# Kernel tuning notes

Hardware: AMD Instinct MI355X
Metric: run time of the kernel (lower is better)

The kernel has to match this reference:

```python
import jax, jax.numpy as jnp
import numpy as np

GRAPH_BIAS_SCALE = 0.7
COMMITMENT_COST = 0.25
DECAY = 0.995
EPS = 1e-6

N_TOKENS = 32768
LATENT = 512
N_SYMBOLS = 8192
EMBED_DIM = 2 * LATENT


def setup_inputs() -> dict:
    key = jax.random.key(0)
    ks = jax.random.split(key, 6)
    return {
        "z_real": jax.random.normal(ks[0], (N_TOKENS, LATENT), jnp.float32),
        "z_imag": jax.random.normal(ks[1], (N_TOKENS, LATENT), jnp.float32),
        "prev_symbol_idx": jax.random.randint(ks[2], (N_TOKENS,), 0, N_SYMBOLS, jnp.int64),
        "codebook": jax.random.normal(ks[3], (N_SYMBOLS, EMBED_DIM), jnp.float32),
        "cluster_size": jax.random.uniform(ks[4], (N_SYMBOLS,), jnp.float32),
        "embed_avg": jax.random.normal(ks[5], (N_SYMBOLS, EMBED_DIM), jnp.float32),
        "adjacency": jax.random.normal(jax.random.fold_in(key, 7), (N_SYMBOLS, N_SYMBOLS), jnp.float32),
    }


def reference(z_real, z_imag, prev_symbol_idx, codebook, cluster_size, embed_avg, adjacency):
    n_symbols = codebook.shape[0]
    z_flat = jnp.concatenate([z_real, z_imag], axis=-1)  # [N, 2*latent]

    # squared-distance matrix via matmul expansion: [N, n_symbols]
    d = (jnp.sum(z_flat ** 2, axis=1, keepdims=True)
         + jnp.sum(codebook ** 2, axis=1)
         - 2.0 * z_flat @ codebook.T)

    # graph-adjacency prior bias (row gather + sigmoid)
    bias = GRAPH_BIAS_SCALE * jax.nn.sigmoid(adjacency[prev_symbol_idx])
    d = d - bias

    min_indices = jnp.argmin(d, axis=1)          # [N]
    z_q = codebook[min_indices]                  # gather, pre-EMA codebook

    # --- EMA codebook update (training mode), scatter via segment_sum ---
    ones = jnp.ones(min_indices.shape, jnp.float32)
    counts = jax.ops.segment_sum(ones, min_indices, num_segments=n_symbols)
    new_cluster_size = cluster_size * DECAY + counts * (1.0 - DECAY)
    embed_sum = jax.ops.segment_sum(jax.lax.stop_gradient(z_flat), min_indices,
                                    num_segments=n_symbols)
    new_embed_avg = embed_avg * DECAY + embed_sum * (1.0 - DECAY)
    n_total = jnp.sum(new_cluster_size)
    cs = (new_cluster_size + EPS) / (n_total + n_symbols * EPS) * n_total
    new_codebook = new_embed_avg / cs[:, None]

    # --- losses and straight-through estimator ---
    loss_vq = jnp.mean((z_q - jax.lax.stop_gradient(z_flat)) ** 2)
    loss_commit = jnp.mean((jax.lax.stop_gradient(z_q) - z_flat) ** 2)
    loss = loss_vq + COMMITMENT_COST * loss_commit

    z_q_st = z_flat + jax.lax.stop_gradient(z_q - z_flat)
    D = z_real.shape[-1]
    z_complex = jax.lax.complex(z_q_st[..., :D], z_q_st[..., D:])

    return z_complex, loss, min_indices, new_codebook, new_cluster_size, new_embed_avg
```

## Files before the change

kernel.cpp:

```cpp
#include <hip/hip_runtime.h>
#include <math.h>
#include <float.h>

#define M_TOK   32768
#define NSYM    8192
#define KDIM    1024
#define LAT     512

#define DECAY_F 0.995f
#define OMD_F   0.005f
#define GBS_F   0.7f
#define EPS_F   1e-6f
#define WIN_F   3.0f

typedef unsigned short u16;
typedef unsigned int   u32;
typedef short short8 __attribute__((ext_vector_type(8)));
typedef float f32x4  __attribute__((ext_vector_type(4)));

#define GLOAD_LDS16(g, l) \
    __builtin_amdgcn_global_load_lds((const __attribute__((address_space(1))) u32*)(g), \
                                     (__attribute__((address_space(3))) u32*)(l), 16, 0, 0)

__device__ __forceinline__ u16 f2bf(float f) {
    u32 u = __float_as_uint(f);
    return (u16)((u + 0x7FFF + ((u >> 16) & 1)) >> 16);
}

__global__ void k_convA(const float* __restrict__ zr, const float* __restrict__ zi,
                        u16* __restrict__ A) {
    size_t t = (size_t)blockIdx.x * 256 + threadIdx.x;
    size_t base = t * 8;
    int tok = (int)(base >> 10);
    int k0  = (int)(base & 1023);
    const float* src = (k0 < 512) ? zr + (size_t)tok * 512 + k0
                                  : zi + (size_t)tok * 512 + (k0 - 512);
    float4 f0 = *(const float4*)src;
    float4 f1 = *(const float4*)(src + 4);
    u32 q0 = f2bf(f0.x) | ((u32)f2bf(f0.y) << 16);
    u32 q1 = f2bf(f0.z) | ((u32)f2bf(f0.w) << 16);
    u32 q2 = f2bf(f1.x) | ((u32)f2bf(f1.y) << 16);
    u32 q3 = f2bf(f1.z) | ((u32)f2bf(f1.w) << 16);
    *(uint4*)&A[base] = make_uint4(q0, q1, q2, q3);
}

__global__ void k_convB(const float* __restrict__ cb, u16* __restrict__ B,
                        float* __restrict__ cnorm) {
    size_t t = (size_t)blockIdx.x * 256 + threadIdx.x;
    size_t base = t * 8;
    float4 f0 = *(const float4*)&cb[base];
    float4 f1 = *(const float4*)&cb[base + 4];
    u32 q0 = f2bf(f0.x) | ((u32)f2bf(f0.y) << 16);
    u32 q1 = f2bf(f0.z) | ((u32)f2bf(f0.w) << 16);
    u32 q2 = f2bf(f1.x) | ((u32)f2bf(f1.y) << 16);
    u32 q3 = f2bf(f1.z) | ((u32)f2bf(f1.w) << 16);
    *(uint4*)&B[base] = make_uint4(q0, q1, q2, q3);
    float nrm = f0.x * f0.x + f0.y * f0.y + f0.z * f0.z + f0.w * f0.w
              + f1.x * f1.x + f1.y * f1.y + f1.z * f1.z + f1.w * f1.w;
#pragma unroll
    for (int m = 32; m; m >>= 1) nrm += __shfl_xor(nrm, m, 64);
    __shared__ float part[4];
    int lane = threadIdx.x & 63, w = threadIdx.x >> 6;
    if (lane == 0) part[w] = nrm;
    __syncthreads();
    if (threadIdx.x == 0)   cnorm[blockIdx.x * 2]     = part[0] + part[1];
    if (threadIdx.x == 128) cnorm[blockIdx.x * 2 + 1] = part[2] + part[3];
}

__global__ __launch_bounds__(256, 4) void k_screen(
    const u16* __restrict__ Ah, const u16* __restrict__ Bh,
    const float* __restrict__ cnorm,
    float* __restrict__ candV, u16* __restrict__ candI)
{
    __shared__ __align__(16) unsigned char smA[16384];
    __shared__ __align__(16) unsigned char smB[16384];
    __shared__ float smv[128][2][2];
    __shared__ float smi[128][2];

    const int sblk = (blockIdx.x & 7) * 128 + (blockIdx.x >> 3);
    const int bx = sblk >> 2;
    const int by = sblk & 3;

    const int tid  = threadIdx.x;
    const int lane = tid & 63;
    const int w    = tid >> 6;
    const int wr   = w >> 1, wc = w & 1;
    const int row0 = bx * 128;
    const int sBase = w * 256;

    for (int cc = 0; cc < 16; ++cc) {
        const int chunk = by * 16 + cc;
        const int colBase = chunk * 128;

        f32x4 acc[4][4];
#pragma unroll
        for (int m = 0; m < 4; ++m)
#pragma unroll
            for (int n = 0; n < 4; ++n) acc[m][n] = (f32x4){0.f, 0.f, 0.f, 0.f};

        for (int ks = 0; ks < 16; ++ks) {
            const int kk0 = ks * 64;
            __syncthreads();
#pragma unroll
            for (int i = 0; i < 4; ++i) {
                int slot = sBase + i * 64 + lane;
                int r = slot >> 3;
                int c = (slot & 7) ^ (r & 7);
                const u16* ga = Ah + ((size_t)(row0 + r) * KDIM + kk0 + c * 8);
                GLOAD_LDS16(ga, smA + (size_t)(sBase + i * 64) * 16);
                const u16* gb = Bh + ((size_t)(colBase + r) * KDIM + kk0 + c * 8);
                GLOAD_LDS16(gb, smB + (size_t)(sBase + i * 64) * 16);
            }
            __syncthreads();
#pragma unroll
            for (int h = 0; h < 2; ++h) {
                short8 af[4], bfr[4];
#pragma unroll
                for (int m = 0; m < 4; ++m) {
                    int r = wr * 64 + m * 16 + (lane & 15);
                    int byte = r * 128 + h * 64 + (lane >> 4) * 16;
                    byte ^= (r & 7) << 4;
                    af[m] = *(const short8*)(smA + byte);
                }
#pragma unroll
                for (int n = 0; n < 4; ++n) {
                    int r = wc * 64 + n * 16 + (lane & 15);
                    int byte = r * 128 + h * 64 + (lane >> 4) * 16;
                    byte ^= (r & 7) << 4;
                    bfr[n] = *(const short8*)(smB + byte);
                }
#pragma unroll
                for (int m = 0; m < 4; ++m)
#pragma unroll
                    for (int n = 0; n < 4; ++n)
                        acc[m][n] = __builtin_amdgcn_mfma_f32_16x16x32_bf16(
                            af[m], bfr[n], acc[m][n], 0, 0, 0);
            }
        }

        float cn[4];
#pragma unroll
        for (int n = 0; n < 4; ++n)
            cn[n] = cnorm[colBase + wc * 64 + n * 16 + (lane & 15)];

#pragma unroll
        for (int m = 0; m < 4; ++m)
#pragma unroll
            for (int j = 0; j < 4; ++j) {
                int rowL = wr * 64 + m * 16 + (lane >> 4) * 4 + j;
                float v1 = INFINITY, v2 = INFINITY, i1v = 0.f;
#pragma unroll
                for (int n = 0; n < 4; ++n) {
                    float s = cn[n] - 2.0f * acc[m][n][j];
                    float ci = (float)(colBase + wc * 64 + n * 16 + (lane & 15));
                    if (s < v1) { v2 = v1; v1 = s; i1v = ci; }
                    else v2 = fminf(v2, s);
                }
#pragma unroll
                for (int msk = 1; msk < 16; msk <<= 1) {
                    float o1 = __shfl_xor(v1, msk, 16);
                    float oi = __shfl_xor(i1v, msk, 16);
                    float o2 = __shfl_xor(v2, msk, 16);
                    float n2 = fminf(fminf(v2, o2), fmaxf(v1, o1));
                    if (o1 < v1) { v1 = o1; i1v = oi; }
                    v2 = n2;
                }
                if ((lane & 15) == 0) {
                    smv[rowL][wc][0] = v1;  smv[rowL][wc][1] = v2;
                    smi[rowL][wc] = i1v;
                }
            }
        __syncthreads();
        {
            int half = tid >> 7;
            int row  = tid & 127;
            float v1 = smv[row][half][0], v2 = smv[row][half][1];
            float iv = smi[row][half];
            size_t tcol = (size_t)(row0 + row);
            int halfIdx = chunk * 2 + half;
            candV[(size_t)(halfIdx * 2 + 0) * M_TOK + tcol] = v1;
            candV[(size_t)(halfIdx * 2 + 1) * M_TOK + tcol] = v2;
            candI[(size_t)halfIdx * M_TOK + tcol]           = (u16)iv;
        }
    }
}

__global__ void k_zero(u32* __restrict__ counts, u32* __restrict__ cursors,
                       float* __restrict__ out_loss) {
    int i = blockIdx.x * 256 + threadIdx.x;
    if (i < NSYM) { counts[i] = 0; cursors[i] = 0; }
    if (i == 0) out_loss[0] = 0.0f;
}

#define SEL_TOK 32
__device__ __forceinline__ void rescore(
    const float* __restrict__ codebook, const float* __restrict__ adjacency,
    const double* zreg, int prw, int col, int lane, double& bestS, int& bestI)
{
    const float* crow = codebook + (size_t)col * KDIM;
    double dot = 0.0, cn2 = 0.0;
#pragma unroll
    for (int j = 0; j < 16; ++j) {
        double c = (double)crow[lane + 64 * j];
        dot += c * zreg[j]; cn2 += c * c;
    }
#pragma unroll
    for (int m = 32; m; m >>= 1) {
        dot += __shfl_xor(dot, m, 64);
        cn2 += __shfl_xor(cn2, m, 64);
    }
    double a = (double)adjacency[(size_t)prw * NSYM + col];
    double sc = cn2 - 2.0 * dot - (double)GBS_F / (1.0 + exp(-a));
    if (sc < bestS || (sc == bestS && col < bestI)) { bestS = sc; bestI = col; }
}

__global__ __launch_bounds__(256) void k_select(
    const float* __restrict__ zr, const float* __restrict__ zi,
    const int* __restrict__ prev,
    const float* __restrict__ codebook,
    const float* __restrict__ adjacency,
    const float* __restrict__ candV, const u16* __restrict__ candI,
    float* __restrict__ out_idx, u32* __restrict__ counts)
{
    __shared__ float sv[256][SEL_TOK + 1];
    __shared__ u16   si[128][SEL_TOK + 2];
    const int tok0 = blockIdx.x * SEL_TOK;
    const int w = threadIdx.x >> 6, lane = threadIdx.x & 63;

    for (int idx = threadIdx.x; idx < 256 * SEL_TOK; idx += 256) {
        int e = idx >> 5, t = idx & (SEL_TOK - 1);
        sv[e][t] = candV[(size_t)e * M_TOK + tok0 + t];
    }
    for (int idx = threadIdx.x; idx < 128 * SEL_TOK; idx += 256) {
        int e = idx >> 5, t = idx & (SEL_TOK - 1);
        si[e][t] = candI[(size_t)e * M_TOK + tok0 + t];
    }
    __syncthreads();

    for (int tt = 0; tt < SEL_TOK / 4; ++tt) {
        const int t = w * (SEL_TOK / 4) + tt;
        const int tok = tok0 + t;
        float va1 = sv[4 * lane + 0][t];
        float va2 = sv[4 * lane + 1][t];
        float vb1 = sv[4 * lane + 2][t];
        float vb2 = sv[4 * lane + 3][t];
        int   ia  = (int)si[2 * lane + 0][t];
        int   ib  = (int)si[2 * lane + 1][t];

        float mm = fminf(va1, vb1);
#pragma unroll
        for (int m = 32; m; m >>= 1) mm = fminf(mm, __shfl_xor(mm, m, 64));
        const float thr = mm + WIN_F;

        unsigned long long m1a = __ballot(va1 <= thr);
        unsigned long long m1b = __ballot(vb1 <= thr);
        unsigned long long mha = __ballot(va2 <= thr);
        unsigned long long mhb = __ballot(vb2 <= thr);

        int bestI;
        if ((mha | mhb) == 0 && __popcll(m1a) + __popcll(m1b) == 1) {
            if (m1a) bestI = __shfl(ia, __ffsll(m1a) - 1, 64);
            else     bestI = __shfl(ib, __ffsll(m1b) - 1, 64);
        } else {
            double zreg[16];
#pragma unroll
            for (int j = 0; j < 8; ++j)
                zreg[j] = (double)zr[(size_t)tok * LAT + lane + 64 * j];
#pragma unroll
            for (int j = 0; j < 8; ++j)
                zreg[8 + j] = (double)zi[(size_t)tok * LAT + lane + 64 * j];
            const int prw = prev[tok];

            double bestS = DBL_MAX; bestI = 0x7FFFFFFF;
            unsigned long long sa = m1a & ~mha, sb = m1b & ~mhb;
            while (sa) { int c = __ffsll(sa) - 1; sa &= sa - 1;
                rescore(codebook, adjacency, zreg, prw, __shfl(ia, c, 64), lane, bestS, bestI); }
            while (sb) { int c = __ffsll(sb) - 1; sb &= sb - 1;
                rescore(codebook, adjacency, zreg, prw, __shfl(ib, c, 64), lane, bestS, bestI); }
            while (mha) { int c = __ffsll(mha) - 1; mha &= mha - 1;
                for (int q = 0; q < 64; ++q)
                    rescore(codebook, adjacency, zreg, prw, c * 128 + q, lane, bestS, bestI); }
            while (mhb) { int c = __ffsll(mhb) - 1; mhb &= mhb - 1;
                for (int q = 0; q < 64; ++q)
                    rescore(codebook, adjacency, zreg, prw, c * 128 + 64 + q, lane, bestS, bestI); }
        }
        if (lane == 0) {
            out_idx[tok] = (float)bestI;
            atomicAdd(&counts[bestI], 1u);
        }
    }
}

__global__ __launch_bounds__(1024) void k_scan(
    const u32* __restrict__ counts, const float* __restrict__ cs_old,
    float* __restrict__ out_cs, u32* __restrict__ offsets,
    float* __restrict__ scal)
{
    const int tid = threadIdx.x;
    const int lane = tid & 63, w = tid >> 6;
    const int base = tid * 8;
    u32 c[8], pre[8], T = 0;
#pragma unroll
    for (int q = 0; q < 8; ++q) { c[q] = counts[base + q]; pre[q] = T; T += c[q]; }
    u32 inc = T;
#pragma unroll
    for (int d = 1; d < 64; d <<= 1) {
        u32 v = __shfl_up(inc, d, 64);
        if (lane >= d) inc += v;
    }
    __shared__ u32 wt[16];
    if (lane == 63) wt[w] = inc;
    __syncthreads();
    if (tid < 16) {
        u32 v = wt[tid];
#pragma unroll
        for (int d = 1; d < 16; d <<= 1) {
            u32 o = __shfl_up(v, d, 16);
            if (tid >= d) v += o;
        }
        wt[tid] = v;
    }
    __syncthreads();
    u32 ex = (w ? wt[w - 1] : 0) + inc - T;
#pragma unroll
    for (int q = 0; q < 8; ++q) offsets[base + q] = ex + pre[q];

    float nt = 0.0f;
#pragma unroll
    for (int q = 0; q < 8; ++q) {
        float ncs = cs_old[base + q] * DECAY_F + OMD_F * (float)c[q];
        out_cs[base + q] = ncs;
        nt += ncs;
    }
#pragma unroll
    for (int m = 32; m; m >>= 1) nt += __shfl_xor(nt, m, 64);
    __shared__ float red[16];
    if (lane == 0) red[w] = nt;
    __syncthreads();
    if (tid == 0) {
        float s = 0.0f;
#pragma unroll
        for (int i = 0; i < 16; ++i) s += red[i];
        scal[0] = s;
        scal[1] = s + (float)NSYM * EPS_F;
    }
}

__global__ void k_place(const float* __restrict__ idxf, const u32* __restrict__ offsets,
                        u32* __restrict__ cursors, u32* __restrict__ list) {
    int t = blockIdx.x * 256 + threadIdx.x;
    int s = (int)idxf[t];
    u32 slot = atomicAdd(&cursors[s], 1u);
    list[offsets[s] + slot] = (u32)t;
}

__global__ __launch_bounds__(256) void k_emit(
    const float* __restrict__ zr, const float* __restrict__ zi,
    const float* __restrict__ embed_avg,
    const u32* __restrict__ counts, const u32* __restrict__ offsets,
    const u32* __restrict__ list, const float* __restrict__ out_cs,
    const float* __restrict__ scal,
    float* __restrict__ out_ea, float* __restrict__ out_cb)
{
    const int s = blockIdx.x;
    const u32 cnt = counts[s], off = offsets[s];
    const int j = threadIdx.x * 4;
    float a0 = 0.f, a1 = 0.f, a2 = 0.f, a3 = 0.f;
    for (u32 n = 0; n < cnt; ++n) {
        int t = (int)list[off + n];
        const float* src = (j < 512) ? zr + (size_t)t * 512 + j
                                     : zi + (size_t)t * 512 + (j - 512);
        float4 v = *(const float4*)src;
        a0 += v.x; a1 += v.y; a2 += v.z; a3 += v.w;
    }
    float4 ea = *(const float4*)&embed_avg[(size_t)s * KDIM + j];
    float4 nea = make_float4(ea.x * DECAY_F + a0 * OMD_F,
                             ea.y * DECAY_F + a1 * OMD_F,
                             ea.z * DECAY_F + a2 * OMD_F,
                             ea.w * DECAY_F + a3 * OMD_F);
    *(float4*)&out_ea[(size_t)s * KDIM + j] = nea;
    float ntot = scal[0], denom = scal[1];
    float cs = (out_cs[s] + EPS_F) / denom * ntot;
    float inv = 1.0f / cs;
    *(float4*)&out_cb[(size_t)s * KDIM + j] =
        make_float4(nea.x * inv, nea.y * inv, nea.z * inv, nea.w * inv);
}

__global__ __launch_bounds__(256) void k_zq(
    const float* __restrict__ zr, const float* __restrict__ zi,
    const float* __restrict__ codebook, const float* __restrict__ idxf,
    float* __restrict__ out_zc, float* __restrict__ out_loss, int interleaved)
{
    const int w = threadIdx.x >> 6, lane = threadIdx.x & 63;
    const int tok = blockIdx.x * 4 + w;
    const int mi = (int)idxf[tok];
    const int j0 = lane * 8;
    float4 re0 = *(const float4*)&codebook[(size_t)mi * KDIM + j0];
    float4 re1 = *(const float4*)&codebook[(size_t)mi * KDIM + j0 + 4];
    float4 im0 = *(const float4*)&codebook[(size_t)mi * KDIM + LAT + j0];
    float4 im1 = *(const float4*)&codebook[(size_t)mi * KDIM + LAT + j0 + 4];
    float4 zr0 = *(const float4*)&zr[(size_t)tok * LAT + j0];
    float4 zr1 = *(const float4*)&zr[(size_t)tok * LAT + j0 + 4];
    float4 zi0 = *(const float4*)&zi[(size_t)tok * LAT + j0];
    float4 zi1 = *(const float4*)&zi[(size_t)tok * LAT + j0 + 4];
    if (interleaved) {
        float2* dst = (float2*)out_zc + (size_t)tok * LAT + j0;
        dst[0] = make_float2(re0.x, im0.x); dst[1] = make_float2(re0.y, im0.y);
        dst[2] = make_float2(re0.z, im0.z); dst[3] = make_float2(re0.w, im0.w);
        dst[4] = make_float2(re1.x, im1.x); dst[5] = make_float2(re1.y, im1.y);
        dst[6] = make_float2(re1.z, im1.z); dst[7] = make_float2(re1.w, im1.w);
    } else {
        *(float4*)&out_zc[(size_t)tok * LAT + j0]     = re0;
        *(float4*)&out_zc[(size_t)tok * LAT + j0 + 4] = re1;
    }
    float l = 0.f;
    l += (re0.x-zr0.x)*(re0.x-zr0.x) + (re0.y-zr0.y)*(re0.y-zr0.y)
       + (re0.z-zr0.z)*(re0.z-zr0.z) + (re0.w-zr0.w)*(re0.w-zr0.w);
    l += (re1.x-zr1.x)*(re1.x-zr1.x) + (re1.y-zr1.y)*(re1.y-zr1.y)
       + (re1.z-zr1.z)*(re1.z-zr1.z) + (re1.w-zr1.w)*(re1.w-zr1.w);
    l += (im0.x-zi0.x)*(im0.x-zi0.x) + (im0.y-zi0.y)*(im0.y-zi0.y)
       + (im0.z-zi0.z)*(im0.z-zi0.z) + (im0.w-zi0.w)*(im0.w-zi0.w);
    l += (im1.x-zi1.x)*(im1.x-zi1.x) + (im1.y-zi1.y)*(im1.y-zi1.y)
       + (im1.z-zi1.z)*(im1.z-zi1.z) + (im1.w-zi1.w)*(im1.w-zi1.w);
#pragma unroll
    for (int m = 32; m; m >>= 1) l += __shfl_xor(l, m, 64);
    if (lane == 0) atomicAdd(out_loss, l);
}

__global__ void k_fin(float* __restrict__ out_loss) {
    out_loss[0] = out_loss[0] * 1.25f / 33554432.0f;
}

extern "C" void kernel_launch(void* const* d_in, const int* in_sizes, int n_in,
                              void* d_out, int out_size, void* d_ws, size_t ws_size,
                              hipStream_t stream) {
    const float* z_real     = (const float*)d_in[0];
    const float* z_imag     = (const float*)d_in[1];
    const int*   prev_idx   = (const int*)d_in[2];
    const float* codebook   = (const float*)d_in[3];
    const float* cluster_sz = (const float*)d_in[4];
    const float* embed_avg  = (const float*)d_in[5];
    const float* adjacency  = (const float*)d_in[6];

    float* out = (float*)d_out;

    const size_t REST = 1 + (size_t)M_TOK + (size_t)NSYM * KDIM + NSYM
                      + (size_t)NSYM * KDIM;
    size_t zc_n = (size_t)out_size - REST;
    const size_t n_z = (size_t)M_TOK * LAT;
    int interleaved = (zc_n >= 2 * n_z) ? 1 : 0;

    float* out_zc   = out;
    float* out_loss = out + zc_n;
    float* out_idx  = out + zc_n + 1;
    float* out_cb   = out + zc_n + 1 + M_TOK;
    float* out_cs   = out_cb + (size_t)NSYM * KDIM;
    float* out_ea   = out_cs + NSYM;

    u16*   A_hi  = (u16*)out_zc;
    u16*   B_hi  = (u16*)out_cb;
    float* cnorm = out_cb + 4194304;
    float* candV = out_ea;
    u16*   candI = (u16*)(out_cb + 4202496);

    u32*   counts  = (u32*)out_zc;
    u32*   cursors = counts + NSYM;
    u32*   offsets = cursors + NSYM;
    u32*   list    = offsets + NSYM;
    float* scal    = (float*)(list + M_TOK);

    k_convA<<<16384, 256, 0, stream>>>(z_real, z_imag, A_hi);
    k_convB<<<4096, 256, 0, stream>>>(codebook, B_hi, cnorm);
    k_screen<<<1024, 256, 0, stream>>>(A_hi, B_hi, cnorm, candV, candI);
    k_zero<<<32, 256, 0, stream>>>(counts, cursors, out_loss);
    k_select<<<M_TOK / SEL_TOK, 256, 0, stream>>>(z_real, z_imag, prev_idx,
                                                  codebook, adjacency,
                                                  candV, candI, out_idx, counts);
    k_scan<<<1, 1024, 0, stream>>>(counts, cluster_sz, out_cs, offsets, scal);
    k_place<<<M_TOK / 256, 256, 0, stream>>>(out_idx, offsets, cursors, list);
    k_emit<<<NSYM, 256, 0, stream>>>(z_real, z_imag, embed_avg, counts, offsets,
                                     list, out_cs, scal, out_ea, out_cb);
    k_zq<<<M_TOK / 4, 256, 0, stream>>>(z_real, z_imag, codebook, out_idx,
                                        out_zc, out_loss, interleaved);
    k_fin<<<1, 1, 0, stream>>>(out_loss);
}
```

Measured before the change: 1.502 ms.

## Split candidate selection into fast path and queued block-parallel exact rescore

Token selection now runs in two kernels. A fast kernel resolves tokens whose bf16 screen yields a single clear candidate and appends every other token to a global work queue. A slow kernel then rescoring each queued token in FP64 with a whole block, spreading its candidate list over four wavefronts instead of one wave doing the work serially, and falls back to a full codebook scan when there are too many candidates. The screening window is also narrowed from 3.0 to 2.5, which cuts rescoring work but makes it more likely that the true argmin is excluded by bf16 screening error.

```diff
diff --git a/kernel.cpp b/kernel.cpp
--- a/kernel.cpp
+++ b/kernel.cpp
@@ -11,7 +11,7 @@
 #define OMD_F   0.005f
 #define GBS_F   0.7f
 #define EPS_F   1e-6f
-#define WIN_F   3.0f
+#define WIN_F   2.5f
 
 typedef unsigned short u16;
 typedef unsigned int   u32;
@@ -186,41 +186,17 @@
 }
 
 __global__ void k_zero(u32* __restrict__ counts, u32* __restrict__ cursors,
-                       float* __restrict__ out_loss) {
+                       u32* __restrict__ qcount, float* __restrict__ out_loss) {
     int i = blockIdx.x * 256 + threadIdx.x;
     if (i < NSYM) { counts[i] = 0; cursors[i] = 0; }
-    if (i == 0) out_loss[0] = 0.0f;
+    if (i == 0) { out_loss[0] = 0.0f; qcount[0] = 0; }
 }
 
 #define SEL_TOK 32
-__device__ __forceinline__ void rescore(
-    const float* __restrict__ codebook, const float* __restrict__ adjacency,
-    const double* zreg, int prw, int col, int lane, double& bestS, int& bestI)
-{
-    const float* crow = codebook + (size_t)col * KDIM;
-    double dot = 0.0, cn2 = 0.0;
-#pragma unroll
-    for (int j = 0; j < 16; ++j) {
-        double c = (double)crow[lane + 64 * j];
-        dot += c * zreg[j]; cn2 += c * c;
-    }
-#pragma unroll
-    for (int m = 32; m; m >>= 1) {
-        dot += __shfl_xor(dot, m, 64);
-        cn2 += __shfl_xor(cn2, m, 64);
-    }
-    double a = (double)adjacency[(size_t)prw * NSYM + col];
-    double sc = cn2 - 2.0 * dot - (double)GBS_F / (1.0 + exp(-a));
-    if (sc < bestS || (sc == bestS && col < bestI)) { bestS = sc; bestI = col; }
-}
-
-__global__ __launch_bounds__(256) void k_select(
-    const float* __restrict__ zr, const float* __restrict__ zi,
-    const int* __restrict__ prev,
-    const float* __restrict__ codebook,
-    const float* __restrict__ adjacency,
+__global__ __launch_bounds__(256) void k_select_fast(
     const float* __restrict__ candV, const u16* __restrict__ candI,
-    float* __restrict__ out_idx, u32* __restrict__ counts)
+    float* __restrict__ out_idx, u32* __restrict__ counts,
+    u32* __restrict__ qcount, u32* __restrict__ queue)
 {
     __shared__ float sv[256][SEL_TOK + 1];
     __shared__ u16   si[128][SEL_TOK + 2];
@@ -244,8 +220,6 @@
         float va2 = sv[4 * lane + 1][t];
         float vb1 = sv[4 * lane + 2][t];
         float vb2 = sv[4 * lane + 3][t];
-        int   ia  = (int)si[2 * lane + 0][t];
-        int   ib  = (int)si[2 * lane + 1][t];
 
         float mm = fminf(va1, vb1);
 #pragma unroll
@@ -254,40 +228,122 @@
 
         unsigned long long m1a = __ballot(va1 <= thr);
         unsigned long long m1b = __ballot(vb1 <= thr);
-        unsigned long long mha = __ballot(va2 <= thr);
-        unsigned long long mhb = __ballot(vb2 <= thr);
-
-        int bestI;
-        if ((mha | mhb) == 0 && __popcll(m1a) + __popcll(m1b) == 1) {
-            if (m1a) bestI = __shfl(ia, __ffsll(m1a) - 1, 64);
-            else     bestI = __shfl(ib, __ffsll(m1b) - 1, 64);
-        } else {
-            double zreg[16];
-#pragma unroll
-            for (int j = 0; j < 8; ++j)
-                zreg[j] = (double)zr[(size_t)tok * LAT + lane + 64 * j];
-#pragma unroll
-            for (int j = 0; j < 8; ++j)
-                zreg[8 + j] = (double)zi[(size_t)tok * LAT + lane + 64 * j];
-            const int prw = prev[tok];
-
-            double bestS = DBL_MAX; bestI = 0x7FFFFFFF;
-            unsigned long long sa = m1a & ~mha, sb = m1b & ~mhb;
-            while (sa) { int c = __ffsll(sa) - 1; sa &= sa - 1;
-                rescore(codebook, adjacency, zreg, prw, __shfl(ia, c, 64), lane, bestS, bestI); }
-            while (sb) { int c = __ffsll(sb) - 1; sb &= sb - 1;
-                rescore(codebook, adjacency, zreg, prw, __shfl(ib, c, 64), lane, bestS, bestI); }
-            while (mha) { int c = __ffsll(mha) - 1; mha &= mha - 1;
-                for (int q = 0; q < 64; ++q)
-                    rescore(codebook, adjacency, zreg, prw, c * 128 + q, lane, bestS, bestI); }
-            while (mhb) { int c = __ffsll(mhb) - 1; mhb &= mhb - 1;
-                for (int q = 0; q < 64; ++q)
-                    rescore(codebook, adjacency, zreg, prw, c * 128 + 64 + q, lane, bestS, bestI); }
-        }
-        if (lane == 0) {
-            out_idx[tok] = (float)bestI;
-            atomicAdd(&counts[bestI], 1u);
-        }
+        unsigned long long mh  = __ballot(va2 <= thr) | __ballot(vb2 <= thr);
+
+        if (mh == 0 && __popcll(m1a) + __popcll(m1b) == 1) {
+            int bestI;
+            if (m1a) { int c = __ffsll(m1a) - 1; bestI = (int)((u16)__shfl((int)si[2*lane+0][t], c, 64)); }
+            else     { int c = __ffsll(m1b) - 1; bestI = (int)((u16)__shfl((int)si[2*lane+1][t], c, 64)); }
+            if (lane == 0) {
+                out_idx[tok] = (float)bestI;
+                atomicAdd(&counts[bestI], 1u);
+            }
+        } else if (lane == 0) {
+            u32 q = atomicAdd(qcount, 1u);
+            queue[q] = (u32)tok;
+        }
+    }
+}
+
+#define MAXC 384
+__global__ __launch_bounds__(256) void k_select_slow(
+    const float* __restrict__ zr, const float* __restrict__ zi,
+    const int* __restrict__ prev,
+    const float* __restrict__ codebook,
+    const float* __restrict__ adjacency,
+    const float* __restrict__ candV, const u16* __restrict__ candI,
+    const u32* __restrict__ qcount, const u32* __restrict__ queue,
+    float* __restrict__ out_idx, u32* __restrict__ counts)
+{
+    __shared__ double zd[KDIM];
+    __shared__ float v1h[128], v2h[128];
+    __shared__ u16   i1h[128];
+    __shared__ int   collist[MAXC];
+    __shared__ int   nsing_sh, nh_sh, scanall_sh;
+    __shared__ int   halves[128];
+    __shared__ double wsc[4];
+    __shared__ int    wix[4];
+    __shared__ float  mm_sh;
+
+    const int tid = threadIdx.x;
+    const int w = tid >> 6, lane = tid & 63;
+    const u32 nq = qcount[0];
+
+    for (u32 qi = blockIdx.x; qi < nq; qi += gridDim.x) {
+        const int tok = (int)queue[qi];
+
+        if (tid < 128) {
+            v1h[tid] = candV[(size_t)(tid * 2 + 0) * M_TOK + tok];
+            v2h[tid] = candV[(size_t)(tid * 2 + 1) * M_TOK + tok];
+            i1h[tid] = candI[(size_t)tid * M_TOK + tok];
+        }
+        for (int k = tid; k < LAT; k += 256) {
+            zd[k]       = (double)zr[(size_t)tok * LAT + k];
+            zd[LAT + k] = (double)zi[(size_t)tok * LAT + k];
+        }
+        if (tid == 0) { nsing_sh = 0; nh_sh = 0; scanall_sh = 0; }
+        __syncthreads();
+
+        if (tid < 64) {
+            float m = fminf(v1h[tid], v1h[tid + 64]);
+#pragma unroll
+            for (int s = 32; s; s >>= 1) m = fminf(m, __shfl_xor(m, s, 64));
+            if (tid == 0) mm_sh = m;
+        }
+        __syncthreads();
+        const float thr = mm_sh + WIN_F;
+
+        if (tid < 128) {
+            bool hs = (v2h[tid] <= thr);
+            if (hs) { int p = atomicAdd(&nh_sh, 1); halves[p] = tid; }
+            else if (v1h[tid] <= thr) { int p = atomicAdd(&nsing_sh, 1); collist[p] = (int)i1h[tid]; }
+        }
+        __syncthreads();
+        int nsing = nsing_sh, nh = nh_sh;
+        int nc = nsing + nh * 64;
+        if (nc > MAXC) { if (tid == 0) scanall_sh = 1; nc = nsing; }
+        __syncthreads();
+        if (!scanall_sh) {
+            for (int h = 0; h < nh; ++h) {
+                if (tid < 64) collist[nsing + h * 64 + tid] = halves[h] * 64 + tid;
+            }
+            nc = nsing + nh * 64;
+        }
+        __syncthreads();
+
+        const int prw = prev[tok];
+        double bestS = DBL_MAX; int bestI = 0x7FFFFFFF;
+        const int total = scanall_sh ? NSYM : nc;
+        for (int ci = w; ci < total; ci += 4) {
+            int col = scanall_sh ? ci : collist[ci];
+            const float* crow = codebook + (size_t)col * KDIM;
+            double dot = 0.0, cn2 = 0.0;
+#pragma unroll
+            for (int j = 0; j < 16; ++j) {
+                double c = (double)crow[lane + 64 * j];
+                dot += c * zd[lane + 64 * j]; cn2 += c * c;
+            }
+#pragma unroll
+            for (int s = 32; s; s >>= 1) {
+                dot += __shfl_xor(dot, s, 64);
+                cn2 += __shfl_xor(cn2, s, 64);
+            }
+            double a = (double)adjacency[(size_t)prw * NSYM + col];
+            double sc = cn2 - 2.0 * dot - (double)GBS_F / (1.0 + exp(-a));
+            if (sc < bestS || (sc == bestS && col < bestI)) { bestS = sc; bestI = col; }
+        }
+        if (lane == 0) { wsc[w] = bestS; wix[w] = bestI; }
+        __syncthreads();
+        if (tid == 0) {
+            double bs = wsc[0]; int bi = wix[0];
+#pragma unroll
+            for (int q = 1; q < 4; ++q) {
+                if (wsc[q] < bs || (wsc[q] == bs && wix[q] < bi)) { bs = wsc[q]; bi = wix[q]; }
+            }
+            out_idx[tok] = (float)bi;
+            atomicAdd(&counts[bi], 1u);
+        }
+        __syncthreads();
     }
 }
 
@@ -468,14 +524,18 @@
     u32*   offsets = cursors + NSYM;
     u32*   list    = offsets + NSYM;
     float* scal    = (float*)(list + M_TOK);
+    u32*   qcount  = (u32*)(scal + 2);
+    u32*   queue   = qcount + 1;
 
     k_convA<<<16384, 256, 0, stream>>>(z_real, z_imag, A_hi);
     k_convB<<<4096, 256, 0, stream>>>(codebook, B_hi, cnorm);
     k_screen<<<1024, 256, 0, stream>>>(A_hi, B_hi, cnorm, candV, candI);
-    k_zero<<<32, 256, 0, stream>>>(counts, cursors, out_loss);
-    k_select<<<M_TOK / SEL_TOK, 256, 0, stream>>>(z_real, z_imag, prev_idx,
-                                                  codebook, adjacency,
-                                                  candV, candI, out_idx, counts);
+    k_zero<<<32, 256, 0, stream>>>(counts, cursors, qcount, out_loss);
+    k_select_fast<<<M_TOK / SEL_TOK, 256, 0, stream>>>(candV, candI, out_idx,
+                                                       counts, qcount, queue);
+    k_select_slow<<<1024, 256, 0, stream>>>(z_real, z_imag, prev_idx, codebook,
+                                            adjacency, candV, candI,
+                                            qcount, queue, out_idx, counts);
     k_scan<<<1, 1024, 0, stream>>>(counts, cluster_sz, out_cs, offsets, scal);
     k_place<<<M_TOK / 256, 256, 0, stream>>>(out_idx, offsets, cursors, list);
     k_emit<<<NSYM, 256, 0, stream>>>(z_real, z_imag, embed_avg, counts, offsets,
```

After: 1.644 ms. +9.5%, slower.
